# Kernel tuning notes

Hardware: AMD Instinct MI355X
Metric: run time of the kernel (lower is better)

## Reference

```python
import jax, jax.numpy as jnp
import numpy as np

B, N, K = 8, 2048, 1024
MAXITER = 5


def hat(w):
    x, y, z = w[..., 0], w[..., 1], w[..., 2]
    O = jnp.zeros_like(x)
    return jnp.stack([
        jnp.stack([O, -z, y], -1),
        jnp.stack([z, O, -x], -1),
        jnp.stack([-y, x, O], -1)], -2)


def se3_exp(x):
    # x [..., 6] twist (w, v) -> [..., 4, 4] rigid transform
    w, v = x[..., :3], x[..., 3:]
    t = jnp.linalg.norm(w, axis=-1)
    small = t < 1e-6
    ts = jnp.where(small, 1.0, t)
    A = jnp.where(small, 1.0 - t * t / 6.0, jnp.sin(ts) / ts)
    Bc = jnp.where(small, 0.5 - t * t / 24.0, (1.0 - jnp.cos(ts)) / (ts * ts))
    Cc = jnp.where(small, 1.0 / 6.0 - t * t / 120.0, (ts - jnp.sin(ts)) / (ts ** 3))
    W = hat(w)
    W2 = W @ W
    I = jnp.eye(3, dtype=x.dtype)
    R = I + A[..., None, None] * W + Bc[..., None, None] * W2
    V = I + Bc[..., None, None] * W + Cc[..., None, None] * W2
    p = jnp.einsum('...ij,...j->...i', V, v)
    top = jnp.concatenate([R, p[..., None]], -1)              # [...,3,4]
    bot = jnp.zeros(top.shape[:-2] + (1, 4), x.dtype).at[..., 0, 3].set(1.0)
    return jnp.concatenate([top, bot], -2)


def transform(g, p):
    # g [...,4,4], p [...,n,3]
    R, t = g[..., :3, :3], g[..., :3, 3]
    return jnp.einsum('...ij,...nj->...ni', R, p) + t[..., None, :]


def encode(p, W1, b1, W2, b2, W3, b3):
    # shared-MLP PointNet 3->64->128->1024 + max pool over points
    h = jax.nn.relu(p @ W1 + b1)
    h = jax.nn.relu(h @ W2 + b2)
    h = h @ W3 + b3
    return h.max(axis=-2)


def setup_inputs() -> dict:
    key = jax.random.key(0)
    ks = jax.random.split(key, 8)
    inp = {
        'p_src': jax.random.normal(ks[0], (B, N, 3), jnp.float32),
        'p_tgt': jax.random.normal(ks[1], (B, N, 3), jnp.float32),
        'igt_twist': 0.1 * jax.random.normal(ks[2], (B, 6), jnp.float32),
        'dt': 0.01 * jnp.ones((1, 6), jnp.float32),
        'W1': jax.random.normal(ks[3], (3, 64), jnp.float32) / np.sqrt(3.0),
        'b1': jnp.zeros((64,), jnp.float32),
        'W2': jax.random.normal(ks[4], (64, 128), jnp.float32) / np.sqrt(64.0),
        'b2': jnp.zeros((128,), jnp.float32),
        'W3': jax.random.normal(ks[5], (128, 1024), jnp.float32) / np.sqrt(128.0),
        'b3': jnp.zeros((1024,), jnp.float32),
    }
    return inp


def reference(p_src, p_tgt, igt_twist, dt, W1, b1, W2, b2, W3, b3):
    bsz = p_src.shape[0]
    dtype = p_src.dtype
    eye4 = jnp.eye(4, dtype=dtype)

    # zero-mean normalization (p0 = target, p1 = source)
    p0_m = p_tgt.mean(axis=1)                     # [B,3]
    p1_m = p_src.mean(axis=1)
    q0 = p_tgt - p0_m[:, None, :]
    q1 = p_src - p1_m[:, None, :]
    a0 = jnp.tile(eye4, (bsz, 1, 1)).at[:, :3, 3].set(p0_m)
    a1 = jnp.tile(eye4, (bsz, 1, 1)).at[:, :3, 3].set(-p1_m)

    f0 = encode(q0, W1, b1, W2, b2, W3, b3)       # [B,K]

    # finite-difference Jacobian of feature wrt 6 twist params
    dtb = jnp.broadcast_to(dt, (bsz, 6))
    twists = -dtb[:, :, None] * jnp.eye(6, dtype=dtype)     # [B,6,6]
    transf = se3_exp(twists)                                 # [B,6,4,4]
    pj = transform(transf, q0[:, None, :, :])                # [B,6,N,3]
    fj = encode(pj, W1, b1, W2, b2, W3, b3)                  # [B,6,K]
    J = (f0[:, :, None] - jnp.swapaxes(fj, 1, 2)) / dtb[:, None, :]   # [B,K,6]

    Jt = jnp.swapaxes(J, 1, 2)                               # [B,6,K]
    H = Jt @ J                                               # [B,6,6]
    pinv = jnp.linalg.inv(H) @ Jt                            # [B,6,K]

    # IC Gauss-Newton iterations (fixed maxiter; xtol early-stop omitted for jit)
    g = jnp.tile(eye4, (bsz, 1, 1))
    r = None
    for _ in range(MAXITER):
        p = transform(g, q1)                                 # [B,N,3]
        f1 = encode(p, W1, b1, W2, b2, W3, b3)
        r = f1 - f0                                          # [B,K]
        dx = -jnp.einsum('bik,bk->bi', pinv, r)              # [B,6]
        g = se3_exp(dx) @ g

    est_g = a0 @ g @ a1                                      # undo zero-mean

    igt = se3_exp(igt_twist)
    loss_pp_wise = jnp.mean(jnp.abs(
        transform(est_g, p_src) - transform(jnp.linalg.inv(igt), p_src)))
    return r, loss_pp_wise
```

## Files before the change

### kernel.cpp

```cpp
#include <hip/hip_runtime.h>
#include <math.h>

#define BATCH 8
#define NPTS 2048
#define KF 1024

typedef _Float16 f16x8 __attribute__((ext_vector_type(8)));
typedef float f32x4 __attribute__((ext_vector_type(4)));

#define MFMA16(a,b,c) __builtin_amdgcn_mfma_f32_16x16x32_f16((a),(b),(c),0,0,0)

#define FSCALE 256.0f
#define INV16  (1.0f/65536.0f)

__device__ __forceinline__ void split_f16s(float x, _Float16& hi, _Float16& lo) {
  float xs = x * FSCALE;
  hi = (_Float16)xs;
  lo = (_Float16)(xs - (float)hi);
}

__device__ __forceinline__ void mat3mul(const float* A, const float* Bm, float* C) {
#pragma unroll
  for (int i = 0; i < 3; ++i)
#pragma unroll
    for (int j = 0; j < 3; ++j)
      C[i*3+j] = A[i*3+0]*Bm[0*3+j] + A[i*3+1]*Bm[1*3+j] + A[i*3+2]*Bm[2*3+j];
}

__device__ void se3_exp_dev(const float* x, float* R, float* p) {
  float wx = x[0], wy = x[1], wz = x[2];
  float vx = x[3], vy = x[4], vz = x[5];
  float t2 = wx*wx + wy*wy + wz*wz;
  float t = sqrtf(t2);
  float A, Bc, Cc;
  if (t < 1e-6f) {
    A  = 1.f - t2*(1.f/6.f);
    Bc = 0.5f - t2*(1.f/24.f);
    Cc = (1.f/6.f) - t2*(1.f/120.f);
  } else {
    float s = sinf(t), c = cosf(t);
    A  = s / t;
    Bc = (1.f - c) / t2;
    Cc = (t - s) / (t2 * t);
  }
  float W[9]  = {0.f, -wz, wy,  wz, 0.f, -wx,  -wy, wx, 0.f};
  float W2[9];
  mat3mul(W, W, W2);
#pragma unroll
  for (int i = 0; i < 9; ++i) {
    float I = (i == 0 || i == 4 || i == 8) ? 1.f : 0.f;
    R[i] = I + A*W[i] + Bc*W2[i];
  }
  float V[9];
#pragma unroll
  for (int i = 0; i < 9; ++i) {
    float I = (i == 0 || i == 4 || i == 8) ? 1.f : 0.f;
    V[i] = I + Bc*W[i] + Cc*W2[i];
  }
  p[0] = V[0]*vx + V[1]*vy + V[2]*vz;
  p[1] = V[3]*vx + V[4]*vy + V[5]*vz;
  p[2] = V[6]*vx + V[7]*vy + V[8]*vz;
}

__global__ void prep_kernel(
    const float* __restrict__ p_src, const float* __restrict__ p_tgt,
    const float* __restrict__ igt_twist, const float* __restrict__ dt,
    const float* __restrict__ W1, const float* __restrict__ b1,
    const float* __restrict__ W2, const float* __restrict__ W3,
    float* __restrict__ mean_tgt, float* __restrict__ mean_src,
    float* __restrict__ W1eff7, float* __restrict__ b1eff7,
    float* __restrict__ W1effL, float* __restrict__ b1effL,
    float* __restrict__ g_buf, float* __restrict__ igt_inv,
    float* __restrict__ loss_out,
    _Float16* __restrict__ W2h, _Float16* __restrict__ W2l,
    _Float16* __restrict__ W3p) {
  const int blk = blockIdx.x, t = threadIdx.x;
  __shared__ float red[256][3];
  if (blk < 128) {
#pragma unroll
    for (int u = 0; u < 4; ++u) {
      int i = blk*1024 + u*256 + t;
      int k = i >> 10, n = i & 1023;
      _Float16 hi, lo;
      split_f16s(W3[i], hi, lo);
      int nt = n >> 4, col = n & 15;
      int ks3 = k >> 5, rr = k & 31;
      int lane = (rr >> 3)*16 + col, jj = rr & 7;
      size_t base = (size_t)nt*4096;
      W3p[base + ((0*4 + ks3)*64 + lane)*8 + jj] = hi;
      W3p[base + ((1*4 + ks3)*64 + lane)*8 + jj] = lo;
    }
  } else if (blk < 160) {
    int i = (blk - 128)*256 + t;
    int k = i >> 7, n = i & 127;
    _Float16 hi, lo;
    split_f16s(W2[i], hi, lo);
    int nt2 = n >> 4, col = n & 15;
    int ks = k >> 5, rr = k & 31;
    int lane = (rr >> 3)*16 + col, jj = rr & 7;
    int dst = ((nt2*2 + ks)*64 + lane)*8 + jj;
    W2h[dst] = hi; W2l[dst] = lo;
  } else if (blk < 176) {
    int unit = blk - 160;
    int which = unit & 1, b = unit >> 1;
    const float* p = (which ? p_src : p_tgt) + (size_t)b*NPTS*3;
    float* m = (which ? mean_src : mean_tgt) + b*3;
    float s0 = 0.f, s1 = 0.f, s2 = 0.f;
    for (int i = t; i < NPTS; i += 256) {
      s0 += p[i*3+0]; s1 += p[i*3+1]; s2 += p[i*3+2];
    }
    red[t][0] = s0; red[t][1] = s1; red[t][2] = s2;
    __syncthreads();
    for (int s = 128; s > 0; s >>= 1) {
      if (t < s) { red[t][0] += red[t+s][0]; red[t][1] += red[t+s][1]; red[t][2] += red[t+s][2]; }
      __syncthreads();
    }
    if (t == 0) {
      m[0] = red[0][0] * (1.f/NPTS);
      m[1] = red[0][1] * (1.f/NPTS);
      m[2] = red[0][2] * (1.f/NPTS);
    }
  } else {
    for (int i = t; i < BATCH*192;  i += 256) W1effL[i] = W1[i % 192];
    for (int i = t; i < BATCH*64;   i += 256) b1effL[i] = b1[i & 63];
    if (t < 192) W1eff7[t] = W1[t];
    if (t < 64)  b1eff7[t] = b1[t];
    if (t < BATCH*16) {
      int i = t & 15;
      g_buf[t] = (i == 0 || i == 5 || i == 10 || i == 15) ? 1.f : 0.f;
    }
    if (t == 0) *loss_out = 0.f;
    if (t < 6) {
      float tw[6] = {0.f,0.f,0.f,0.f,0.f,0.f};
      tw[t] = -dt[t];
      float R[9], tr[3];
      se3_exp_dev(tw, R, tr);
      float* Wd = W1eff7 + (t+1)*192;
      for (int d = 0; d < 3; ++d)
        for (int c = 0; c < 64; ++c)
          Wd[d*64+c] = R[0*3+d]*W1[c] + R[1*3+d]*W1[64+c] + R[2*3+d]*W1[128+c];
      float* bd = b1eff7 + (t+1)*64;
      for (int c = 0; c < 64; ++c)
        bd[c] = b1[c] + tr[0]*W1[c] + tr[1]*W1[64+c] + tr[2]*W1[128+c];
    }
    if (t >= 32 && t < 32+BATCH) {
      int b = t - 32;
      float R[9], tr[3];
      se3_exp_dev(igt_twist + b*6, R, tr);
      float* inv = igt_inv + b*12;
      for (int r = 0; r < 3; ++r) {
        inv[r*4+0] = R[0*3+r];
        inv[r*4+1] = R[1*3+r];
        inv[r*4+2] = R[2*3+r];
        inv[r*4+3] = -(R[0*3+r]*tr[0] + R[1*3+r]*tr[1] + R[2*3+r]*tr[2]);
      }
    }
  }
}

__device__ __forceinline__ f32x4 zero4() {
  f32x4 z; z[0]=0.f; z[1]=0.f; z[2]=0.f; z[3]=0.f; return z;
}

__device__ __forceinline__ void l12_ptile(
    float px, float py, float pz,
    const float* __restrict__ w1, const float* __restrict__ bb1,
    const _Float16* __restrict__ W2h, const _Float16* __restrict__ W2l,
    const float* __restrict__ b2,
    _Float16* scr, int l, int lm, int q,
    f16x8 (&A3h)[4], f16x8 (&A3l)[4]) {
  f16x8 A2h[2], A2l[2];
#pragma unroll
  for (int ks = 0; ks < 2; ++ks) {
    const int c0 = ks*32 + q*8;
    float wa[8], wb[8], wc[8], bv[8];
    *(float4*)&wa[0] = *(const float4*)(w1 + c0);
    *(float4*)&wa[4] = *(const float4*)(w1 + c0 + 4);
    *(float4*)&wb[0] = *(const float4*)(w1 + 64 + c0);
    *(float4*)&wb[4] = *(const float4*)(w1 + 64 + c0 + 4);
    *(float4*)&wc[0] = *(const float4*)(w1 + 128 + c0);
    *(float4*)&wc[4] = *(const float4*)(w1 + 128 + c0 + 4);
    *(float4*)&bv[0] = *(const float4*)(bb1 + c0);
    *(float4*)&bv[4] = *(const float4*)(bb1 + c0 + 4);
#pragma unroll
    for (int jj = 0; jj < 8; ++jj) {
      float h = fmaf(px, wa[jj], fmaf(py, wb[jj], fmaf(pz, wc[jj], bv[jj])));
      h = fmaxf(h, 0.f);
      _Float16 hi, lo;
      split_f16s(h, hi, lo);
      A2h[ks][jj] = hi; A2l[ks][jj] = lo;
    }
  }
#pragma unroll
  for (int nt2 = 0; nt2 < 8; ++nt2) {
    f32x4 acc = zero4();
#pragma unroll
    for (int ks = 0; ks < 2; ++ks) {
      const int base = ((nt2*2 + ks)*64 + l)*8;
      const f16x8 Bh = *(const f16x8*)(W2h + base);
      const f16x8 Bl = *(const f16x8*)(W2l + base);
      acc = MFMA16(A2l[ks], Bh, acc);
      acc = MFMA16(A2h[ks], Bl, acc);
      acc = MFMA16(A2h[ks], Bh, acc);
    }
    const int c2 = nt2*16 + lm;
    const float b2v = b2[c2];
    const int ks3 = c2 >> 5;
    const int k31 = c2 & 31;
    const int qw = k31 >> 3, jw = k31 & 7;
#pragma unroll
    for (int r = 0; r < 4; ++r) {
      const int mrow = q*4 + r;
      float h = fmaxf(acc[r]*INV16 + b2v, 0.f);
      _Float16 hi, lo;
      split_f16s(h, hi, lo);
      const int idx = (ks3*64 + qw*16 + mrow)*8 + jw;
      scr[idx] = hi;
      scr[2048 + idx] = lo;
    }
  }
#pragma unroll
  for (int ks3 = 0; ks3 < 4; ++ks3) {
    const int base = (ks3*64 + l)*8;
    A3h[ks3] = *(const f16x8*)&scr[base];
    A3l[ks3] = *(const f16x8*)&scr[2048 + base];
  }
}

__global__ __launch_bounds__(256, 2) void encode_big(
    const float* __restrict__ pts, const float* __restrict__ mean,
    const float* __restrict__ W1e, const float* __restrict__ b1e,
    const _Float16* __restrict__ W2h, const _Float16* __restrict__ W2l,
    const _Float16* __restrict__ W3p, const float* __restrict__ b2,
    float* __restrict__ partial) {
  const int t = threadIdx.x;
  const int w = t >> 6, l = t & 63;
  const int lm = l & 15, q = l >> 4;
  const int pblk = blockIdx.x;
  const int j = blockIdx.y;
  const int b = blockIdx.z;

  __shared__ __align__(16) _Float16 smem[16384];

  const int ptbase = pblk*256 + w*64;
  float mx0 = mean[b*3+0], my0 = mean[b*3+1], mz0 = mean[b*3+2];
  const float* w1 = W1e + j*192;
  const float* bb1 = b1e + j*64;

  f16x8 A3h[4][4], A3l[4][4];
  _Float16* scr = smem + w*4096;
#pragma unroll
  for (int p = 0; p < 4; ++p) {
    const float* pp = pts + ((size_t)b*NPTS + ptbase + p*16 + lm)*3;
    l12_ptile(pp[0]-mx0, pp[1]-my0, pp[2]-mz0, w1, bb1, W2h, W2l, b2,
              scr, l, lm, q, A3h[p], A3l[p]);
  }
  __syncthreads();

  float* maxb = (float*)(smem + 8192);
  {
    f16x8 s0 = *(const f16x8*)(W3p + t*8);
    f16x8 s1 = *(const f16x8*)(W3p + 2048 + t*8);
    *(f16x8*)&smem[t*8] = s0;
    *(f16x8*)&smem[2048 + t*8] = s1;
  }
  __syncthreads();

  for (int k = 0; k < 64; ++k) {
    const int cur = (k & 1)*4096;
    const int nxt = cur ^ 4096;
    f16x8 s0, s1;
    const int have_next = (k + 1 < 64);
    if (have_next) {
      const _Float16* src = W3p + (size_t)(k+1)*4096;
      s0 = *(const f16x8*)(src + t*8);
      s1 = *(const f16x8*)(src + 2048 + t*8);
    }
    f16x8 B[2][4];
#pragma unroll
    for (int lev = 0; lev < 2; ++lev)
#pragma unroll
      for (int ks = 0; ks < 4; ++ks)
        B[lev][ks] = *(const f16x8*)&smem[cur + ((lev*4 + ks)*64 + l)*8];

    f32x4 a[4] = {zero4(), zero4(), zero4(), zero4()};
#pragma unroll
    for (int ks = 0; ks < 4; ++ks) {
#pragma unroll
      for (int p = 0; p < 4; ++p) a[p] = MFMA16(A3l[p][ks], B[0][ks], a[p]);
#pragma unroll
      for (int p = 0; p < 4; ++p) a[p] = MFMA16(A3h[p][ks], B[1][ks], a[p]);
#pragma unroll
      for (int p = 0; p < 4; ++p) a[p] = MFMA16(A3h[p][ks], B[0][ks], a[p]);
    }
    float mx = -INFINITY;
#pragma unroll
    for (int p = 0; p < 4; ++p)
#pragma unroll
      for (int r = 0; r < 4; ++r) mx = fmaxf(mx, a[p][r]);
    mx = fmaxf(mx, __shfl_xor(mx, 16, 64));
    mx = fmaxf(mx, __shfl_xor(mx, 32, 64));
    if (l < 16) maxb[w*1024 + k*16 + lm] = mx;

    if (have_next) {
      *(f16x8*)&smem[nxt + t*8] = s0;
      *(f16x8*)&smem[nxt + 2048 + t*8] = s1;
    }
    __syncthreads();
  }
  float* pout = partial + ((size_t)(j*BATCH + b)*8 + pblk)*KF;
  for (int f = t; f < KF; f += 256) {
    float m = fmaxf(fmaxf(maxb[f], maxb[1024+f]), fmaxf(maxb[2048+f], maxb[3072+f]));
    pout[f] = m*INV16;
  }
}

__global__ __launch_bounds__(512) void pinv_kernel(
    const float* __restrict__ partialB, const float* __restrict__ dt,
    float* __restrict__ pinvb, float* __restrict__ feats0) {
  const int b = blockIdx.x, t = threadIdx.x;
  float Jk2[2][6];
  float H[21];
#pragma unroll
  for (int i = 0; i < 21; ++i) H[i] = 0.f;
#pragma unroll
  for (int h = 0; h < 2; ++h) {
    const int kf = t + h*512;
    float fv[7];
#pragma unroll
    for (int j = 0; j < 7; ++j) {
      const float* ps = partialB + ((size_t)(j*BATCH + b)*8)*KF + kf;
      float m = ps[0];
#pragma unroll
      for (int s = 1; s < 8; ++s) m = fmaxf(m, ps[(size_t)s*KF]);
      fv[j] = m;
    }
    feats0[(size_t)b*KF + kf] = fv[0];
#pragma unroll
    for (int i = 0; i < 6; ++i) Jk2[h][i] = (fv[0] - fv[1+i]) / dt[i];
    int idx = 0;
#pragma unroll
    for (int i = 0; i < 6; ++i)
#pragma unroll
      for (int jj = i; jj < 6; ++jj) H[idx++] += Jk2[h][i]*Jk2[h][jj];
  }
#pragma unroll
  for (int i = 0; i < 21; ++i) {
    float v = H[i];
#pragma unroll
    for (int o = 1; o < 64; o <<= 1) v += __shfl_xor(v, o, 64);
    H[i] = v;
  }
  __shared__ float hred[8*21];
  __shared__ float s_hinv[36];
  const int wv = t >> 6, ln = t & 63;
  if (ln == 0)
#pragma unroll
    for (int i = 0; i < 21; ++i) hred[wv*21 + i] = H[i];
  __syncthreads();
  if (t == 0) {
    float Ht[21];
#pragma unroll
    for (int i = 0; i < 21; ++i) {
      float s = 0.f;
#pragma unroll
      for (int w2 = 0; w2 < 8; ++w2) s += hred[w2*21 + i];
      Ht[i] = s;
    }
    double h00=Ht[0], h01=Ht[1], h02=Ht[2], h03=Ht[3], h04=Ht[4], h05=Ht[5];
    double h11=Ht[6], h12=Ht[7], h13=Ht[8], h14=Ht[9], h15=Ht[10];
    double h22=Ht[11], h23=Ht[12], h24=Ht[13], h25=Ht[14];
    double h33=Ht[15], h34=Ht[16], h35=Ht[17];
    double h44=Ht[18], h45=Ht[19];
    double h55=Ht[20];
    double l00=sqrt(h00), i00=1.0/l00;
    double l10=h01*i00, l20=h02*i00, l30=h03*i00, l40=h04*i00, l50=h05*i00;
    double l11=sqrt(h11-l10*l10), i11=1.0/l11;
    double l21=(h12-l20*l10)*i11;
    double l31=(h13-l30*l10)*i11;
    double l41=(h14-l40*l10)*i11;
    double l51=(h15-l50*l10)*i11;
    double l22=sqrt(h22-l20*l20-l21*l21), i22=1.0/l22;
    double l32=(h23-l30*l20-l31*l21)*i22;
    double l42=(h24-l40*l20-l41*l21)*i22;
    double l52=(h25-l50*l20-l51*l21)*i22;
    double l33=sqrt(h33-l30*l30-l31*l31-l32*l32), i33=1.0/l33;
    double l43=(h34-l40*l30-l41*l31-l42*l32)*i33;
    double l53=(h35-l50*l30-l51*l31-l52*l32)*i33;
    double l44=sqrt(h44-l40*l40-l41*l41-l42*l42-l43*l43), i44=1.0/l44;
    double l54=(h45-l50*l40-l51*l41-l52*l42-l53*l43)*i44;
    double l55=sqrt(h55-l50*l50-l51*l51-l52*l52-l53*l53-l54*l54), i55=1.0/l55;
    double m00=i00, m11=i11, m22=i22, m33=i33, m44=i44, m55=i55;
    double m10=-i11*(l10*m00);
    double m20=-i22*(l20*m00+l21*m10);
    double m21=-i22*(l21*m11);
    double m30=-i33*(l30*m00+l31*m10+l32*m20);
    double m31=-i33*(l31*m11+l32*m21);
    double m32=-i33*(l32*m22);
    double m40=-i44*(l40*m00+l41*m10+l42*m20+l43*m30);
    double m41=-i44*(l41*m11+l42*m21+l43*m31);
    double m42=-i44*(l42*m22+l43*m32);
    double m43=-i44*(l43*m33);
    double m50=-i55*(l50*m00+l51*m10+l52*m20+l53*m30+l54*m40);
    double m51=-i55*(l51*m11+l52*m21+l53*m31+l54*m41);
    double m52=-i55*(l52*m22+l53*m32+l54*m42);
    double m53=-i55*(l53*m33+l54*m43);
    double m54=-i55*(l54*m44);
    double v00 = m00*m00+m10*m10+m20*m20+m30*m30+m40*m40+m50*m50;
    double v01 = m10*m11+m20*m21+m30*m31+m40*m41+m50*m51;
    double v02 = m20*m22+m30*m32+m40*m42+m50*m52;
    double v03 = m30*m33+m40*m43+m50*m53;
    double v04 = m40*m44+m50*m54;
    double v05 = m50*m55;
    double v11 = m11*m11+m21*m21+m31*m31+m41*m41+m51*m51;
    double v12 = m21*m22+m31*m32+m41*m42+m51*m52;
    double v13 = m31*m33+m41*m43+m51*m53;
    double v14 = m41*m44+m51*m54;
    double v15 = m51*m55;
    double v22 = m22*m22+m32*m32+m42*m42+m52*m52;
    double v23 = m32*m33+m42*m43+m52*m53;
    double v24 = m42*m44+m52*m54;
    double v25 = m52*m55;
    double v33 = m33*m33+m43*m43+m53*m53;
    double v34 = m43*m44+m53*m54;
    double v35 = m53*m55;
    double v44 = m44*m44+m54*m54;
    double v45 = m54*m55;
    double v55 = m55*m55;
    s_hinv[0]=(float)v00;  s_hinv[1]=(float)v01;  s_hinv[2]=(float)v02;
    s_hinv[3]=(float)v03;  s_hinv[4]=(float)v04;  s_hinv[5]=(float)v05;
    s_hinv[6]=(float)v01;  s_hinv[7]=(float)v11;  s_hinv[8]=(float)v12;
    s_hinv[9]=(float)v13;  s_hinv[10]=(float)v14; s_hinv[11]=(float)v15;
    s_hinv[12]=(float)v02; s_hinv[13]=(float)v12; s_hinv[14]=(float)v22;
    s_hinv[15]=(float)v23; s_hinv[16]=(float)v24; s_hinv[17]=(float)v25;
    s_hinv[18]=(float)v03; s_hinv[19]=(float)v13; s_hinv[20]=(float)v23;
    s_hinv[21]=(float)v33; s_hinv[22]=(float)v34; s_hinv[23]=(float)v35;
    s_hinv[24]=(float)v04; s_hinv[25]=(float)v14; s_hinv[26]=(float)v24;
    s_hinv[27]=(float)v34; s_hinv[28]=(float)v44; s_hinv[29]=(float)v45;
    s_hinv[30]=(float)v05; s_hinv[31]=(float)v15; s_hinv[32]=(float)v25;
    s_hinv[33]=(float)v35; s_hinv[34]=(float)v45; s_hinv[35]=(float)v55;
  }
  __syncthreads();
#pragma unroll
  for (int h = 0; h < 2; ++h) {
    const int kf = t + h*512;
#pragma unroll
    for (int i = 0; i < 6; ++i) {
      float s = 0.f;
#pragma unroll
      for (int jj = 0; jj < 6; ++jj) s += s_hinv[i*6+jj] * Jk2[h][jj];
      pinvb[((size_t)b*6 + i)*KF + kf] = s;
    }
  }
}

__global__ __launch_bounds__(256, 3) void encode_loop(
    const float* __restrict__ pts, const float* __restrict__ mean,
    const float* __restrict__ W1e, const float* __restrict__ b1e,
    const _Float16* __restrict__ W2h, const _Float16* __restrict__ W2l,
    const _Float16* __restrict__ W3p, const float* __restrict__ b2,
    float* __restrict__ partial2) {
  const int t = threadIdx.x;
  const int w = t >> 6, l = t & 63;
  const int lm = l & 15, q = l >> 4;
  const int pblk = blockIdx.x;
  const int fg = blockIdx.y;
  const int b = blockIdx.z;
  const int nt0 = fg*16;

  __shared__ __align__(16) _Float16 smem[16384];

  const int pt = pblk*64 + w*16;
  float mx0 = mean[b*3+0], my0 = mean[b*3+1], mz0 = mean[b*3+2];
  const float* w1 = W1e + b*192;
  const float* bb1 = b1e + b*64;

  f16x8 A3h[4], A3l[4];
  {
    const float* pp = pts + ((size_t)b*NPTS + pt + lm)*3;
    l12_ptile(pp[0]-mx0, pp[1]-my0, pp[2]-mz0, w1, bb1, W2h, W2l, b2,
              smem + w*4096, l, lm, q, A3h, A3l);
  }
  __syncthreads();

  float* maxb = (float*)(smem + 8192);
  {
    const _Float16* src = W3p + (size_t)nt0*4096;
    f16x8 s0 = *(const f16x8*)(src + t*8);
    f16x8 s1 = *(const f16x8*)(src + 2048 + t*8);
    *(f16x8*)&smem[t*8] = s0;
    *(f16x8*)&smem[2048 + t*8] = s1;
  }
  __syncthreads();

  for (int k = 0; k < 16; ++k) {
    const int cur = (k & 1)*4096;
    const int nxt = cur ^ 4096;
    f16x8 s0, s1;
    const int have_next = (k + 1 < 16);
    if (have_next) {
      const _Float16* src = W3p + (size_t)(nt0 + k + 1)*4096;
      s0 = *(const f16x8*)(src + t*8);
      s1 = *(const f16x8*)(src + 2048 + t*8);
    }
    f16x8 B[2][4];
#pragma unroll
    for (int lev = 0; lev < 2; ++lev)
#pragma unroll
      for (int ks = 0; ks < 4; ++ks)
        B[lev][ks] = *(const f16x8*)&smem[cur + ((lev*4 + ks)*64 + l)*8];

    f32x4 a = zero4();
#pragma unroll
    for (int ks = 0; ks < 4; ++ks) {
      a = MFMA16(A3l[ks], B[0][ks], a);
      a = MFMA16(A3h[ks], B[1][ks], a);
      a = MFMA16(A3h[ks], B[0][ks], a);
    }
    float mx = fmaxf(fmaxf(a[0], a[1]), fmaxf(a[2], a[3]));
    mx = fmaxf(mx, __shfl_xor(mx, 16, 64));
    mx = fmaxf(mx, __shfl_xor(mx, 32, 64));
    if (l < 16) maxb[w*256 + k*16 + lm] = mx;

    if (have_next) {
      *(f16x8*)&smem[nxt + t*8] = s0;
      *(f16x8*)&smem[nxt + 2048 + t*8] = s1;
    }
    __syncthreads();
  }
  if (t < 256) {
    float m = fmaxf(fmaxf(maxb[t], maxb[256+t]), fmaxf(maxb[512+t], maxb[768+t]));
    partial2[((size_t)b*32 + pblk)*KF + fg*256 + t] = m*INV16;
  }
}

__global__ __launch_bounds__(1024) void update_kernel(
    const float* __restrict__ feats0, const float* __restrict__ partial2,
    const float* __restrict__ pinv, float* __restrict__ g_buf,
    const float* __restrict__ W1, const float* __restrict__ b1,
    float* __restrict__ W1effL, float* __restrict__ b1effL,
    float* __restrict__ r_out,
    const float* __restrict__ mean_tgt, const float* __restrict__ mean_src,
    const float* __restrict__ p_src, const float* __restrict__ igt_inv,
    float* __restrict__ loss_out, int final_it) {
  const int b = blockIdx.x, t = threadIdx.x;
  const float* ps = partial2 + (size_t)b*32*KF + t;
  float m = ps[0];
#pragma unroll
  for (int s = 1; s < 32; ++s) m = fmaxf(m, ps[(size_t)s*KF]);
  float r = m - feats0[(size_t)b*KF + t];
  r_out[(size_t)b*KF + t] = r;
  float acc[6];
#pragma unroll
  for (int i = 0; i < 6; ++i) acc[i] = pinv[((size_t)b*6+i)*KF + t] * r;
#pragma unroll
  for (int i = 0; i < 6; ++i) {
    float v = acc[i];
#pragma unroll
    for (int o = 1; o < 64; o <<= 1) v += __shfl_xor(v, o, 64);
    acc[i] = v;
  }
  __shared__ float wred[16*6];
  const int wv = t >> 6, ln = t & 63;
  if (ln == 0)
#pragma unroll
    for (int i = 0; i < 6; ++i) wred[wv*6 + i] = acc[i];
  __syncthreads();
  __shared__ float s_g[16];
  __shared__ float s_e[12];
  __shared__ float s_v[12];
  if (t == 0) {
    float dx[6];
    for (int i = 0; i < 6; ++i) {
      float s = 0.f;
      for (int w2 = 0; w2 < 16; ++w2) s += wred[w2*6 + i];
      dx[i] = -s;
    }
    float R[9], p[3];
    se3_exp_dev(dx, R, p);
    float* g = g_buf + b*16;
    float gn[16];
    for (int r2 = 0; r2 < 3; ++r2)
      for (int c = 0; c < 4; ++c)
        gn[r2*4+c] = R[r2*3+0]*g[c] + R[r2*3+1]*g[4+c] + R[r2*3+2]*g[8+c] + p[r2]*g[12+c];
    gn[12] = 0.f; gn[13] = 0.f; gn[14] = 0.f; gn[15] = 1.f;
    for (int i = 0; i < 16; ++i) { g[i] = gn[i]; s_g[i] = gn[i]; }
    if (final_it) {
      const float* p0m = mean_tgt + b*3;
      const float* p1m = mean_src + b*3;
      for (int r2 = 0; r2 < 3; ++r2) {
        s_e[r2*4+0] = gn[r2*4+0];
        s_e[r2*4+1] = gn[r2*4+1];
        s_e[r2*4+2] = gn[r2*4+2];
        s_e[r2*4+3] = gn[r2*4+3]
                    - (gn[r2*4+0]*p1m[0] + gn[r2*4+1]*p1m[1] + gn[r2*4+2]*p1m[2])
                    + p0m[r2];
      }
    }
  }
  if (final_it && t >= 64 && t < 76) s_v[t-64] = igt_inv[b*12 + (t-64)];
  __syncthreads();
  if (!final_it) {
    if (t < 192) {
      int d = t >> 6, c = t & 63;
      W1effL[b*192 + t] = s_g[0*4+d]*W1[c] + s_g[1*4+d]*W1[64+c] + s_g[2*4+d]*W1[128+c];
    } else if (t < 256) {
      int i = t - 192;
      b1effL[b*64 + i] = b1[i] + s_g[3]*W1[i] + s_g[7]*W1[64+i] + s_g[11]*W1[128+i];
    }
  } else {
    float ls = 0.f;
    for (int n = t; n < NPTS; n += 1024) {
      const float* p = p_src + ((size_t)b*NPTS + n)*3;
      float px = p[0], py = p[1], pz = p[2];
#pragma unroll
      for (int r2 = 0; r2 < 3; ++r2) {
        float d1 = s_e[r2*4+0]*px + s_e[r2*4+1]*py + s_e[r2*4+2]*pz + s_e[r2*4+3];
        float d2 = s_v[r2*4+0]*px + s_v[r2*4+1]*py + s_v[r2*4+2]*pz + s_v[r2*4+3];
        ls += fabsf(d1 - d2);
      }
    }
#pragma unroll
    for (int o = 1; o < 64; o <<= 1) ls += __shfl_xor(ls, o, 64);
    __shared__ float lred[16];
    if (ln == 0) lred[wv] = ls;
    __syncthreads();
    if (t == 0) {
      float s = 0.f;
      for (int w2 = 0; w2 < 16; ++w2) s += lred[w2];
      atomicAdd(loss_out, s * (1.f/((float)BATCH*NPTS*3)));
    }
  }
}

extern "C" void kernel_launch(void* const* d_in, const int* in_sizes, int n_in,
                              void* d_out, int out_size, void* d_ws, size_t ws_size,
                              hipStream_t stream) {
  const float* p_src     = (const float*)d_in[0];
  const float* p_tgt     = (const float*)d_in[1];
  const float* igt_twist = (const float*)d_in[2];
  const float* dt        = (const float*)d_in[3];
  const float* W1        = (const float*)d_in[4];
  const float* b1        = (const float*)d_in[5];
  const float* W2        = (const float*)d_in[6];
  const float* b2        = (const float*)d_in[7];
  const float* W3        = (const float*)d_in[8];
  float* out = (float*)d_out;

  float* ws = (float*)d_ws;
  float* mean_tgt = ws;  ws += 32;
  float* mean_src = ws;  ws += 32;
  float* W1eff7   = ws;  ws += 7*192;
  float* b1eff7   = ws;  ws += 7*64;
  float* feats0   = ws;  ws += BATCH*KF;
  float* W1effL   = ws;  ws += BATCH*192;
  float* b1effL   = ws;  ws += BATCH*64;
  float* g_buf    = ws;  ws += BATCH*16;
  float* pinvb    = ws;  ws += BATCH*6*KF;
  float* igt_inv  = ws;  ws += 96;
  _Float16* W2h = (_Float16*)ws;  ws += 8192/2;
  _Float16* W2l = (_Float16*)ws;  ws += 8192/2;
  _Float16* W3p = (_Float16*)ws;  ws += 262144/2;
  float* partialB = ws;  ws += 56*8*KF;
  float* partial2 = ws;  ws += BATCH*32*KF;

  float* r_out    = out;
  float* loss_out = out + BATCH*KF;

  prep_kernel<<<dim3(177), 256, 0, stream>>>(
      p_src, p_tgt, igt_twist, dt, W1, b1, W2, W3,
      mean_tgt, mean_src, W1eff7, b1eff7, W1effL, b1effL, g_buf, igt_inv,
      loss_out, W2h, W2l, W3p);

  encode_big<<<dim3(8, 7, BATCH), 256, 0, stream>>>(
      p_tgt, mean_tgt, W1eff7, b1eff7, W2h, W2l, W3p, b2, partialB);
  pinv_kernel<<<dim3(BATCH), 512, 0, stream>>>(partialB, dt, pinvb, feats0);

  for (int it = 0; it < 5; ++it) {
    encode_loop<<<dim3(32, 4, BATCH), 256, 0, stream>>>(
        p_src, mean_src, W1effL, b1effL, W2h, W2l, W3p, b2, partial2);
    update_kernel<<<dim3(BATCH), 1024, 0, stream>>>(
        feats0, partial2, pinvb, g_buf, W1, b1, W1effL, b1effL, r_out,
        mean_tgt, mean_src, p_src, igt_inv, loss_out, (it == 4) ? 1 : 0);
  }
}
```

Baseline: 290.8 us.

## Fuse update into encode_loop via last-block counter and split encode_big over K

```diff
diff --git a/kernel.cpp b/kernel.cpp
--- a/kernel.cpp
+++ b/kernel.cpp
@@ -71,7 +71,7 @@
     float* __restrict__ W1eff7, float* __restrict__ b1eff7,
     float* __restrict__ W1effL, float* __restrict__ b1effL,
     float* __restrict__ g_buf, float* __restrict__ igt_inv,
-    float* __restrict__ loss_out,
+    float* __restrict__ loss_out, int* __restrict__ ctr,
     _Float16* __restrict__ W2h, _Float16* __restrict__ W2l,
     _Float16* __restrict__ W3p) {
   const int blk = blockIdx.x, t = threadIdx.x;
@@ -130,6 +130,7 @@
       g_buf[t] = (i == 0 || i == 5 || i == 10 || i == 15) ? 1.f : 0.f;
     }
     if (t == 0) *loss_out = 0.f;
+    if (t >= 200 && t < 240) ctr[t-200] = 0;
     if (t < 6) {
       float tw[6] = {0.f,0.f,0.f,0.f,0.f,0.f};
       tw[t] = -dt[t];
@@ -236,7 +237,9 @@
   const int t = threadIdx.x;
   const int w = t >> 6, l = t & 63;
   const int lm = l & 15, q = l >> 4;
-  const int pblk = blockIdx.x;
+  const int pblk = blockIdx.x >> 1;
+  const int half = blockIdx.x & 1;
+  const int k0 = half*32;
   const int j = blockIdx.y;
   const int b = blockIdx.z;
 
@@ -259,20 +262,21 @@
 
   float* maxb = (float*)(smem + 8192);
   {
-    f16x8 s0 = *(const f16x8*)(W3p + t*8);
-    f16x8 s1 = *(const f16x8*)(W3p + 2048 + t*8);
+    const _Float16* src = W3p + (size_t)k0*4096;
+    f16x8 s0 = *(const f16x8*)(src + t*8);
+    f16x8 s1 = *(const f16x8*)(src + 2048 + t*8);
     *(f16x8*)&smem[t*8] = s0;
     *(f16x8*)&smem[2048 + t*8] = s1;
   }
   __syncthreads();
 
-  for (int k = 0; k < 64; ++k) {
+  for (int k = 0; k < 32; ++k) {
     const int cur = (k & 1)*4096;
     const int nxt = cur ^ 4096;
     f16x8 s0, s1;
-    const int have_next = (k + 1 < 64);
+    const int have_next = (k + 1 < 32);
     if (have_next) {
-      const _Float16* src = W3p + (size_t)(k+1)*4096;
+      const _Float16* src = W3p + (size_t)(k0 + k + 1)*4096;
       s0 = *(const f16x8*)(src + t*8);
       s1 = *(const f16x8*)(src + 2048 + t*8);
     }
@@ -300,7 +304,7 @@
       for (int r = 0; r < 4; ++r) mx = fmaxf(mx, a[p][r]);
     mx = fmaxf(mx, __shfl_xor(mx, 16, 64));
     mx = fmaxf(mx, __shfl_xor(mx, 32, 64));
-    if (l < 16) maxb[w*1024 + k*16 + lm] = mx;
+    if (l < 16) maxb[w*512 + k*16 + lm] = mx;
 
     if (have_next) {
       *(f16x8*)&smem[nxt + t*8] = s0;
@@ -308,9 +312,9 @@
     }
     __syncthreads();
   }
-  float* pout = partial + ((size_t)(j*BATCH + b)*8 + pblk)*KF;
-  for (int f = t; f < KF; f += 256) {
-    float m = fmaxf(fmaxf(maxb[f], maxb[1024+f]), fmaxf(maxb[2048+f], maxb[3072+f]));
+  float* pout = partial + (((size_t)(j*BATCH + b)*2 + half)*8 + pblk)*512;
+  for (int f = t; f < 512; f += 256) {
+    float m = fmaxf(fmaxf(maxb[f], maxb[512+f]), fmaxf(maxb[1024+f], maxb[1536+f]));
     pout[f] = m*INV16;
   }
 }
@@ -329,10 +333,10 @@
     float fv[7];
 #pragma unroll
     for (int j = 0; j < 7; ++j) {
-      const float* ps = partialB + ((size_t)(j*BATCH + b)*8)*KF + kf;
+      const float* ps = partialB + (((size_t)(j*BATCH + b)*2 + h)*8)*512 + t;
       float m = ps[0];
 #pragma unroll
-      for (int s = 1; s < 8; ++s) m = fmaxf(m, ps[(size_t)s*KF]);
+      for (int s = 1; s < 8; ++s) m = fmaxf(m, ps[s*512]);
       fv[j] = m;
     }
     feats0[(size_t)b*KF + kf] = fv[0];
@@ -459,7 +463,14 @@
     const float* __restrict__ W1e, const float* __restrict__ b1e,
     const _Float16* __restrict__ W2h, const _Float16* __restrict__ W2l,
     const _Float16* __restrict__ W3p, const float* __restrict__ b2,
-    float* __restrict__ partial2) {
+    float* __restrict__ partial2,
+    const float* __restrict__ feats0, const float* __restrict__ pinv,
+    float* __restrict__ g_buf, const float* __restrict__ W1,
+    const float* __restrict__ b1, float* __restrict__ W1effL,
+    float* __restrict__ b1effL, float* __restrict__ r_out,
+    const float* __restrict__ mean_tgt, const float* __restrict__ mean_src,
+    const float* __restrict__ igt_inv, float* __restrict__ loss_out,
+    int* __restrict__ ctr, int final_it) {
   const int t = threadIdx.x;
   const int w = t >> 6, l = t & 63;
   const int lm = l & 15, q = l >> 4;
@@ -528,31 +539,33 @@
     }
     __syncthreads();
   }
-  if (t < 256) {
+  {
     float m = fmaxf(fmaxf(maxb[t], maxb[256+t]), fmaxf(maxb[512+t], maxb[768+t]));
     partial2[((size_t)b*32 + pblk)*KF + fg*256 + t] = m*INV16;
   }
-}
-
-__global__ __launch_bounds__(1024) void update_kernel(
-    const float* __restrict__ feats0, const float* __restrict__ partial2,
-    const float* __restrict__ pinv, float* __restrict__ g_buf,
-    const float* __restrict__ W1, const float* __restrict__ b1,
-    float* __restrict__ W1effL, float* __restrict__ b1effL,
-    float* __restrict__ r_out,
-    const float* __restrict__ mean_tgt, const float* __restrict__ mean_src,
-    const float* __restrict__ p_src, const float* __restrict__ igt_inv,
-    float* __restrict__ loss_out, int final_it) {
-  const int b = blockIdx.x, t = threadIdx.x;
-  const float* ps = partial2 + (size_t)b*32*KF + t;
-  float m = ps[0];
-#pragma unroll
-  for (int s = 1; s < 32; ++s) m = fmaxf(m, ps[(size_t)s*KF]);
-  float r = m - feats0[(size_t)b*KF + t];
-  r_out[(size_t)b*KF + t] = r;
-  float acc[6];
-#pragma unroll
-  for (int i = 0; i < 6; ++i) acc[i] = pinv[((size_t)b*6+i)*KF + t] * r;
+
+  __threadfence();
+  __syncthreads();
+  __shared__ int s_last;
+  if (t == 0) s_last = (atomicAdd(&ctr[b], 1) == 127) ? 1 : 0;
+  __syncthreads();
+  if (!s_last) return;
+  __threadfence();
+
+  const int wv = w, ln = l;
+  float acc[6] = {0.f,0.f,0.f,0.f,0.f,0.f};
+#pragma unroll
+  for (int u = 0; u < 4; ++u) {
+    const int kf = u*256 + t;
+    const float* ps = partial2 + (size_t)b*32*KF + kf;
+    float m = ps[0];
+#pragma unroll
+    for (int s = 1; s < 32; ++s) m = fmaxf(m, ps[(size_t)s*KF]);
+    float r = m - feats0[(size_t)b*KF + kf];
+    r_out[(size_t)b*KF + kf] = r;
+#pragma unroll
+    for (int i = 0; i < 6; ++i) acc[i] += pinv[((size_t)b*6+i)*KF + kf] * r;
+  }
 #pragma unroll
   for (int i = 0; i < 6; ++i) {
     float v = acc[i];
@@ -560,8 +573,7 @@
     for (int o = 1; o < 64; o <<= 1) v += __shfl_xor(v, o, 64);
     acc[i] = v;
   }
-  __shared__ float wred[16*6];
-  const int wv = t >> 6, ln = t & 63;
+  __shared__ float wred[4*6];
   if (ln == 0)
 #pragma unroll
     for (int i = 0; i < 6; ++i) wred[wv*6 + i] = acc[i];
@@ -573,7 +585,7 @@
     float dx[6];
     for (int i = 0; i < 6; ++i) {
       float s = 0.f;
-      for (int w2 = 0; w2 < 16; ++w2) s += wred[w2*6 + i];
+      for (int w2 = 0; w2 < 4; ++w2) s += wred[w2*6 + i];
       dx[i] = -s;
     }
     float R[9], p[3];
@@ -604,14 +616,14 @@
     if (t < 192) {
       int d = t >> 6, c = t & 63;
       W1effL[b*192 + t] = s_g[0*4+d]*W1[c] + s_g[1*4+d]*W1[64+c] + s_g[2*4+d]*W1[128+c];
-    } else if (t < 256) {
+    } else {
       int i = t - 192;
       b1effL[b*64 + i] = b1[i] + s_g[3]*W1[i] + s_g[7]*W1[64+i] + s_g[11]*W1[128+i];
     }
   } else {
     float ls = 0.f;
-    for (int n = t; n < NPTS; n += 1024) {
-      const float* p = p_src + ((size_t)b*NPTS + n)*3;
+    for (int n = t; n < NPTS; n += 256) {
+      const float* p = pts + ((size_t)b*NPTS + n)*3;
       float px = p[0], py = p[1], pz = p[2];
 #pragma unroll
       for (int r2 = 0; r2 < 3; ++r2) {
@@ -622,12 +634,11 @@
     }
 #pragma unroll
     for (int o = 1; o < 64; o <<= 1) ls += __shfl_xor(ls, o, 64);
-    __shared__ float lred[16];
+    __shared__ float lred[4];
     if (ln == 0) lred[wv] = ls;
     __syncthreads();
     if (t == 0) {
-      float s = 0.f;
-      for (int w2 = 0; w2 < 16; ++w2) s += lred[w2];
+      float s = lred[0] + lred[1] + lred[2] + lred[3];
       atomicAdd(loss_out, s * (1.f/((float)BATCH*NPTS*3)));
     }
   }
@@ -658,10 +669,11 @@
   float* g_buf    = ws;  ws += BATCH*16;
   float* pinvb    = ws;  ws += BATCH*6*KF;
   float* igt_inv  = ws;  ws += 96;
+  int*   ctr      = (int*)ws;  ws += 64;
   _Float16* W2h = (_Float16*)ws;  ws += 8192/2;
   _Float16* W2l = (_Float16*)ws;  ws += 8192/2;
   _Float16* W3p = (_Float16*)ws;  ws += 262144/2;
-  float* partialB = ws;  ws += 56*8*KF;
+  float* partialB = ws;  ws += 56*16*512;
   float* partial2 = ws;  ws += BATCH*32*KF;
 
   float* r_out    = out;
@@ -670,17 +682,16 @@
   prep_kernel<<<dim3(177), 256, 0, stream>>>(
       p_src, p_tgt, igt_twist, dt, W1, b1, W2, W3,
       mean_tgt, mean_src, W1eff7, b1eff7, W1effL, b1effL, g_buf, igt_inv,
-      loss_out, W2h, W2l, W3p);
-
-  encode_big<<<dim3(8, 7, BATCH), 256, 0, stream>>>(
+      loss_out, ctr, W2h, W2l, W3p);
+
+  encode_big<<<dim3(16, 7, BATCH), 256, 0, stream>>>(
       p_tgt, mean_tgt, W1eff7, b1eff7, W2h, W2l, W3p, b2, partialB);
   pinv_kernel<<<dim3(BATCH), 512, 0, stream>>>(partialB, dt, pinvb, feats0);
 
   for (int it = 0; it < 5; ++it) {
     encode_loop<<<dim3(32, 4, BATCH), 256, 0, stream>>>(
-        p_src, mean_src, W1effL, b1effL, W2h, W2l, W3p, b2, partial2);
-    update_kernel<<<dim3(BATCH), 1024, 0, stream>>>(
-        feats0, partial2, pinvb, g_buf, W1, b1, W1effL, b1effL, r_out,
-        mean_tgt, mean_src, p_src, igt_inv, loss_out, (it == 4) ? 1 : 0);
-  }
-}
+        p_src, mean_src, W1effL, b1effL, W2h, W2l, W3p, b2, partial2,
+        feats0, pinvb, g_buf, W1, b1, W1effL, b1effL, r_out,
+        mean_tgt, mean_src, igt_inv, loss_out, ctr + it*8, (it == 4) ? 1 : 0);
+  }
+}
```

Result: slower. 719.4 us (+147.4%).
